# Kernel tuning notes

Measured on AMD Instinct MI355X. Metric: run time of the kernel, lower is better.

The kernel has to match this reference:

```python
import jax, jax.numpy as jnp
import numpy as np

N_NODES = 50000
N_EDGES = 800000
IN_DIM = 256
OUT_DIM = 256


def setup_inputs() -> dict:
    key = jax.random.key(0)
    k_feat, k_src, k_dst, k_w0, k_w1, k_b = jax.random.split(key, 6)
    feat = jax.random.normal(k_feat, (N_NODES, IN_DIM), dtype=jnp.float32)
    src = jax.random.randint(k_src, (N_EDGES,), 0, N_NODES, dtype=jnp.int64)
    dst = jax.random.randint(k_dst, (N_EDGES,), 0, N_NODES, dtype=jnp.int64)
    # GraphConv weights (Glorot-ish scale) and biases
    W0 = jax.random.normal(k_w0, (IN_DIM, OUT_DIM), dtype=jnp.float32) / np.sqrt(IN_DIM)
    W1 = jax.random.normal(k_w1, (OUT_DIM, OUT_DIM), dtype=jnp.float32) / np.sqrt(OUT_DIM)
    b0 = jnp.zeros((OUT_DIM,), dtype=jnp.float32)
    b1 = jnp.zeros((OUT_DIM,), dtype=jnp.float32)
    # single shared nn.PReLU parameter (torch default init 0.25)
    prelu_a = jnp.asarray(0.25, dtype=jnp.float32)
    return {"feat": feat, "src": src, "dst": dst,
            "W0": W0, "b0": b0, "W1": W1, "b1": b1, "prelu_a": prelu_a}


def _prelu(x, a):
    return jnp.where(x >= 0, x, a * x)


def reference(feat, src, dst, W0, b0, W1, b1, prelu_a):
    N = feat.shape[0]
    ones = jnp.ones((src.shape[0],), dtype=feat.dtype)
    out_deg = jnp.zeros((N,), dtype=feat.dtype).at[src].add(ones)
    in_deg = jnp.zeros((N,), dtype=feat.dtype).at[dst].add(ones)
    # DGL norm='both': clamp degrees to >=1 before rsqrt
    norm_s = jax.lax.rsqrt(jnp.maximum(out_deg, 1.0))[:, None]  # [N,1]
    norm_d = jax.lax.rsqrt(jnp.maximum(in_deg, 1.0))[:, None]   # [N,1]

    def graph_conv(h, W, b):
        # h' = D_in^{-1/2} A (D_out^{-1/2} h) W + b
        msg = (h * norm_s)[src]                                   # [E, d]
        agg = jax.ops.segment_sum(msg, dst, num_segments=N)       # [N, d]
        return (agg * norm_d) @ W + b

    h = _prelu(graph_conv(feat, W0, b0), prelu_a)
    hg = jnp.sum(h, axis=0, keepdims=True)                        # SumPooling [1, d]
    h = _prelu(graph_conv(h, W1, b1), prelu_a)
    hg = jnp.concatenate([hg, jnp.sum(h, axis=0, keepdims=True)], axis=-1)
    return (h, hg)
```

## Files before the change

kernel.cpp:

```cpp
#include <hip/hip_runtime.h>
#include <stdint.h>

#define NN 50000
#define NE 800000
#define DIM 256

#define HB 128
#define HT 512
#define HALF 25000
#define HWORDS 12500

#define NSLICE 8
#define SCH 32
#define NPB 64
#define ECH 2048

#define GB ((NN + 31) / 32)

typedef __bf16 bf16x8 __attribute__((ext_vector_type(8)));
typedef float f32x4 __attribute__((ext_vector_type(4)));
typedef unsigned u32x4 __attribute__((ext_vector_type(4)));
typedef int i32x4 __attribute__((ext_vector_type(4)));

__device__ __forceinline__ unsigned short f2bf(float f) {
  union { float f; unsigned u; } v; v.f = f;
  unsigned r = v.u + 0x7fffu + ((v.u >> 16) & 1u);
  return (unsigned short)(r >> 16);
}

__global__ __launch_bounds__(HT) void hist_kernel(const int* __restrict__ src,
                                                  const int* __restrict__ dst,
                                                  unsigned* __restrict__ Hs,
                                                  unsigned* __restrict__ Hd) {
  __shared__ unsigned lds[HWORDS];
  const int tid = threadIdx.x;
  const int b = blockIdx.x;
#pragma unroll
  for (int phase = 0; phase < 4; ++phase) {
    const int* arr = (phase < 2) ? src : dst;
    unsigned* H = (phase < 2) ? Hs : Hd;
    const int r = phase & 1;
    const int lo = r * HALF;
    for (int w = tid; w < HWORDS; w += HT) lds[w] = 0u;
    __syncthreads();
    for (int e = b * HT + tid; e < NE; e += HB * HT) {
      unsigned local = (unsigned)(arr[e] - lo);
      if (local < (unsigned)HALF)
        atomicAdd(&lds[local >> 1], 1u << ((local & 1) * 16));
    }
    __syncthreads();
    for (int w = tid; w < HWORDS; w += HT)
      H[(size_t)b * HALF + r * HWORDS + w] = lds[w];
    __syncthreads();
  }
}

__global__ void reduce_norm_kernel(const unsigned* __restrict__ Hs,
                                   const unsigned* __restrict__ Hd,
                                   unsigned* __restrict__ Pd,
                                   int* __restrict__ in_cnt,
                                   float* __restrict__ norm_s,
                                   float* __restrict__ norm_d,
                                   float* __restrict__ hg) {
  int w = blockIdx.x * blockDim.x + threadIdx.x;
  if (blockIdx.x == 0) {
    hg[threadIdx.x] = 0.f;
    hg[256 + threadIdx.x] = 0.f;
  }
  if (w >= 2 * HWORDS) return;
  unsigned ss = 0, dd = 0;
  for (int b = 0; b < HB; ++b) {
    Pd[(size_t)b * HALF + w] = dd;
    ss += Hs[(size_t)b * HALF + w];
    dd += Hd[(size_t)b * HALF + w];
  }
  int r = (w >= HWORDS) ? 1 : 0;
  int lw = w - r * HWORDS;
  int n0 = r * HALF + lw * 2;
  unsigned s0 = ss & 0xffffu, s1 = ss >> 16;
  unsigned d0 = dd & 0xffffu, d1 = dd >> 16;
  in_cnt[n0] = (int)d0;
  in_cnt[n0 + 1] = (int)d1;
  norm_s[n0] = rsqrtf(fmaxf((float)s0, 1.0f));
  norm_s[n0 + 1] = rsqrtf(fmaxf((float)s1, 1.0f));
  norm_d[n0] = rsqrtf(fmaxf((float)d0, 1.0f));
  norm_d[n0 + 1] = rsqrtf(fmaxf((float)d1, 1.0f));
}

__global__ __launch_bounds__(1024) void scan_kernel(const int* __restrict__ in_cnt,
                                                    int* __restrict__ row_ptr) {
  __shared__ int wsum[16];
  int tid = threadIdx.x;
  int lane = tid & 63, wave = tid >> 6;
  int carry = 0;
  for (int base = 0; base < NN; base += 4096) {
    int i0 = base + tid * 4;
    int v[4];
#pragma unroll
    for (int j = 0; j < 4; ++j) {
      int i = i0 + j;
      v[j] = (i < NN) ? in_cnt[i] : 0;
    }
    int tsum = v[0] + v[1] + v[2] + v[3];
    int incl = tsum;
#pragma unroll
    for (int off = 1; off < 64; off <<= 1) {
      int t = __shfl_up(incl, off, 64);
      if (lane >= off) incl += t;
    }
    if (lane == 63) wsum[wave] = incl;
    __syncthreads();
    int waveoff = 0;
    for (int w = 0; w < wave; ++w) waveoff += wsum[w];
    int chunk_total = 0;
    for (int w = 0; w < 16; ++w) chunk_total += wsum[w];
    int run = carry + waveoff + (incl - tsum);
#pragma unroll
    for (int j = 0; j < 4; ++j) {
      int i = i0 + j;
      if (i < NN) row_ptr[i] = run;
      run += v[j];
    }
    carry += chunk_total;
    __syncthreads();
  }
  if (tid == 0) row_ptr[NN] = carry;
}

__global__ __launch_bounds__(HT) void fill_kernel(const int* __restrict__ src,
                                                  const int* __restrict__ dst,
                                                  const int* __restrict__ row_ptr,
                                                  const unsigned* __restrict__ Pd,
                                                  int* __restrict__ colx) {
  __shared__ unsigned lds[HWORDS];
  const int tid = threadIdx.x;
  const int b = blockIdx.x;
#pragma unroll
  for (int r = 0; r < 2; ++r) {
    const int lo = r * HALF;
    for (int w = tid; w < HWORDS; w += HT) lds[w] = 0u;
    __syncthreads();
    for (int e = b * HT + tid; e < NE; e += HB * HT) {
      int n = dst[e];
      unsigned local = (unsigned)(n - lo);
      if (local < (unsigned)HALF) {
        int sh = (local & 1) * 16;
        unsigned old = atomicAdd(&lds[local >> 1], 1u << sh);
        unsigned rank = (old >> sh) & 0xffffu;
        unsigned pref = (Pd[(size_t)b * HALF + r * HWORDS + (local >> 1)] >> sh) & 0xffffu;
        colx[row_ptr[n] + (int)pref + (int)rank] = src[e];
      }
    }
    __syncthreads();
  }
}

__device__ __forceinline__ void swizzleW_body(const float* __restrict__ W,
                                              unsigned short* __restrict__ Wb, int idx) {
  int lane = idx & 63;
  int blk = idx >> 6;
  int kc = blk & 7, nt = blk >> 3;
  int kbase = kc * 32 + (lane >> 4) * 8;
  int col = nt * 16 + (lane & 15);
  ushort4 o0, o1;
  o0.x = f2bf(W[(size_t)(kbase + 0) * DIM + col]);
  o0.y = f2bf(W[(size_t)(kbase + 1) * DIM + col]);
  o0.z = f2bf(W[(size_t)(kbase + 2) * DIM + col]);
  o0.w = f2bf(W[(size_t)(kbase + 3) * DIM + col]);
  o1.x = f2bf(W[(size_t)(kbase + 4) * DIM + col]);
  o1.y = f2bf(W[(size_t)(kbase + 5) * DIM + col]);
  o1.z = f2bf(W[(size_t)(kbase + 6) * DIM + col]);
  o1.w = f2bf(W[(size_t)(kbase + 7) * DIM + col]);
  ((ushort4*)Wb)[idx * 2 + 0] = o0;
  ((ushort4*)Wb)[idx * 2 + 1] = o1;
}

__global__ void prep_kernel(const float* __restrict__ feat, const float* __restrict__ norm_s,
                            unsigned short* __restrict__ featb,
                            const float* __restrict__ W0, unsigned short* __restrict__ Wb0,
                            const float* __restrict__ W1, unsigned short* __restrict__ Wb1) {
  int blk = blockIdx.x;
  if (blk < 12500) {
    int i = blk * 256 + threadIdx.x;
    int node = i >> 6;
    int ch4 = i & 63;
    float s = norm_s[node];
    float4 v = ((const float4*)feat)[i];
    ushort4 o;
    o.x = f2bf(v.x * s); o.y = f2bf(v.y * s); o.z = f2bf(v.z * s); o.w = f2bf(v.w * s);
    int sl = ch4 >> 3;
    int w4 = ch4 & 7;
    ((ushort4*)featb)[(size_t)sl * (NN * 8) + (size_t)node * 8 + w4] = o;
  } else if (blk < 12532) {
    swizzleW_body(W0, Wb0, (blk - 12500) * 256 + threadIdx.x);
  } else {
    swizzleW_body(W1, Wb1, (blk - 12532) * 256 + threadIdx.x);
  }
}

__device__ __forceinline__ void acc_row(float* a, u32x4 p) {
  a[0] += __uint_as_float(p.x << 16);
  a[1] += __uint_as_float(p.x & 0xffff0000u);
  a[2] += __uint_as_float(p.y << 16);
  a[3] += __uint_as_float(p.y & 0xffff0000u);
  a[4] += __uint_as_float(p.z << 16);
  a[5] += __uint_as_float(p.z & 0xffff0000u);
  a[6] += __uint_as_float(p.w << 16);
  a[7] += __uint_as_float(p.w & 0xffff0000u);
}

__global__ __launch_bounds__(256) void agg_kernel(const unsigned short* __restrict__ X,
                                                  unsigned short* __restrict__ agg,
                                                  const int* __restrict__ row_ptr,
                                                  const int* __restrict__ colx,
                                                  const float* __restrict__ norm_d) {
  __shared__ int ecol[ECH];
  const int s = blockIdx.x & (NSLICE - 1);
  const int nb = blockIdx.x >> 3;
  const int tid = threadIdx.x;
  const int grp = tid >> 2;
  const int cl = tid & 3;
  const int node = nb * NPB + grp;

  const int nfirst = nb * NPB;
  const int nlast = (nfirst + NPB < NN) ? (nfirst + NPB) : NN;
  const int estart = row_ptr[nfirst];
  const int eend = row_ptr[nlast];

  int e = 0, end = 0;
  if (node < NN) { e = row_ptr[node]; end = row_ptr[node + 1]; }

  const unsigned short* Xs = X + (size_t)s * (NN * SCH);
  const size_t loff = (size_t)cl * 8;

  float a[8];
#pragma unroll
  for (int j = 0; j < 8; ++j) a[j] = 0.f;

  const int base0 = estart & ~3;
  for (int base = base0; base < eend; base += ECH) {
    const int lim = (base + ECH < eend) ? (base + ECH) : eend;
    __syncthreads();
    for (int k = base + tid * 4; k < lim; k += 1024) {
      i32x4 v = __builtin_nontemporal_load((const i32x4*)(colx + k));
      *(i32x4*)&ecol[k - base] = v;
    }
    __syncthreads();
    const int hi = (end < lim) ? end : lim;
    for (; e + 4 <= hi; e += 4) {
      int c0 = ecol[e - base + 0];
      int c1 = ecol[e - base + 1];
      int c2 = ecol[e - base + 2];
      int c3 = ecol[e - base + 3];
      u32x4 r0 = *(const u32x4*)(Xs + (size_t)c0 * SCH + loff);
      u32x4 r1 = *(const u32x4*)(Xs + (size_t)c1 * SCH + loff);
      u32x4 r2 = *(const u32x4*)(Xs + (size_t)c2 * SCH + loff);
      u32x4 r3 = *(const u32x4*)(Xs + (size_t)c3 * SCH + loff);
      acc_row(a, r0);
      acc_row(a, r1);
      acc_row(a, r2);
      acc_row(a, r3);
    }
    for (; e < hi; ++e) {
      int c = ecol[e - base];
      u32x4 r = *(const u32x4*)(Xs + (size_t)c * SCH + loff);
      acc_row(a, r);
    }
  }

  if (node < NN) {
    float nd = norm_d[node];
    u32x4 o;
    o.x = (unsigned)f2bf(a[0] * nd) | ((unsigned)f2bf(a[1] * nd) << 16);
    o.y = (unsigned)f2bf(a[2] * nd) | ((unsigned)f2bf(a[3] * nd) << 16);
    o.z = (unsigned)f2bf(a[4] * nd) | ((unsigned)f2bf(a[5] * nd) << 16);
    o.w = (unsigned)f2bf(a[6] * nd) | ((unsigned)f2bf(a[7] * nd) << 16);
    __builtin_nontemporal_store(o, (u32x4*)(agg + (size_t)node * DIM + (size_t)s * SCH + loff));
  }
}

#define LDSROW 264
#define FROW 260
__global__ __launch_bounds__(256) void gemm_mfma_kernel(const unsigned short* __restrict__ A,
                                                        const unsigned short* __restrict__ Wb,
                                                        const float* __restrict__ bias,
                                                        const float* __restrict__ prelu_a_ptr,
                                                        const float* __restrict__ norm_s,
                                                        float* __restrict__ C,
                                                        unsigned short* __restrict__ Cb,
                                                        float* __restrict__ hg_part) {
  __shared__ unsigned short As[32 * LDSROW];
  int tid = threadIdx.x;
  int r0 = blockIdx.x * 32;
#pragma unroll
  for (int p = 0; p < 4; ++p) {
    int idx = p * 256 + tid;
    int row = idx >> 5;
    int seg = idx & 31;
    int grow = r0 + row;
    ushort4 v0 = {0, 0, 0, 0}, v1 = {0, 0, 0, 0};
    if (grow < NN) {
      const ushort4* g = (const ushort4*)(A + (size_t)grow * DIM + seg * 8);
      v0 = g[0]; v1 = g[1];
    }
    *(ushort4*)(&As[row * LDSROW + seg * 8 + 0]) = v0;
    *(ushort4*)(&As[row * LDSROW + seg * 8 + 4]) = v1;
  }
  __syncthreads();

  int wave = tid >> 6, lane = tid & 63;
  int quad = lane >> 4, l16 = lane & 15;

  f32x4 acc[2][4];
#pragma unroll
  for (int mt = 0; mt < 2; ++mt)
#pragma unroll
    for (int nti = 0; nti < 4; ++nti)
      acc[mt][nti] = (f32x4){0.f, 0.f, 0.f, 0.f};

#pragma unroll
  for (int kc = 0; kc < 8; ++kc) {
    bf16x8 a[2], b[4];
#pragma unroll
    for (int mt = 0; mt < 2; ++mt)
      a[mt] = *(const bf16x8*)(&As[(mt * 16 + l16) * LDSROW + kc * 32 + quad * 8]);
#pragma unroll
    for (int nti = 0; nti < 4; ++nti) {
      int nt = wave * 4 + nti;
      b[nti] = *(const bf16x8*)(Wb + ((size_t)(nt * 8 + kc) * 64 + lane) * 8);
    }
#pragma unroll
    for (int mt = 0; mt < 2; ++mt)
#pragma unroll
      for (int nti = 0; nti < 4; ++nti)
        acc[mt][nti] = __builtin_amdgcn_mfma_f32_16x16x32_bf16(a[mt], b[nti], acc[mt][nti], 0, 0, 0);
  }

  float pa = *prelu_a_ptr;
  float bv[4], cs[4];
#pragma unroll
  for (int nti = 0; nti < 4; ++nti) {
    bv[nti] = bias[wave * 64 + nti * 16 + l16];
    cs[nti] = 0.f;
  }
#pragma unroll
  for (int mt = 0; mt < 2; ++mt) {
#pragma unroll
    for (int nti = 0; nti < 4; ++nti) {
#pragma unroll
      for (int r = 0; r < 4; ++r) {
        int rowg = r0 + mt * 16 + quad * 4 + r;
        float x = acc[mt][nti][r] + bv[nti];
        x = (x >= 0.f) ? x : pa * x;
        acc[mt][nti][r] = x;
        if (rowg < NN) cs[nti] += x;
      }
    }
  }
#pragma unroll
  for (int nti = 0; nti < 4; ++nti) {
    cs[nti] += __shfl_xor(cs[nti], 16, 64);
    cs[nti] += __shfl_xor(cs[nti], 32, 64);
  }
  if (quad == 0) {
#pragma unroll
    for (int nti = 0; nti < 4; ++nti)
      hg_part[(size_t)blockIdx.x * 256 + wave * 64 + nti * 16 + l16] = cs[nti];
  }

  float* LF = (float*)As;
#pragma unroll
  for (int chunk = 0; chunk < 2; ++chunk) {
    __syncthreads();
#pragma unroll
    for (int nti = 0; nti < 4; ++nti) {
      int colw = wave * 64 + nti * 16 + l16;
#pragma unroll
      for (int r = 0; r < 4; ++r)
        LF[(quad * 4 + r) * FROW + colw] = acc[chunk][nti][r];
    }
    __syncthreads();
    int rowbase = r0 + chunk * 16;
    if (C) {
#pragma unroll
      for (int s = 0; s < 4; ++s) {
        int g = s * 256 + tid;
        int row = g >> 6, cg = g & 63;
        int rowg = rowbase + row;
        if (rowg < NN) {
          float4 v = *(const float4*)&LF[row * FROW + cg * 4];
          *(float4*)(C + (size_t)rowg * DIM + cg * 4) = v;
        }
      }
    }
    if (Cb) {
#pragma unroll
      for (int s = 0; s < 2; ++s) {
        int g = s * 256 + tid;
        int row = g >> 5, cg = g & 31;
        int rowg = rowbase + row;
        if (rowg < NN) {
          float ns = norm_s[rowg];
          float4 v0 = *(const float4*)&LF[row * FROW + cg * 8];
          float4 v1 = *(const float4*)&LF[row * FROW + cg * 8 + 4];
          uint4 o;
          o.x = (unsigned)f2bf(v0.x * ns) | ((unsigned)f2bf(v0.y * ns) << 16);
          o.y = (unsigned)f2bf(v0.z * ns) | ((unsigned)f2bf(v0.w * ns) << 16);
          o.z = (unsigned)f2bf(v1.x * ns) | ((unsigned)f2bf(v1.y * ns) << 16);
          o.w = (unsigned)f2bf(v1.z * ns) | ((unsigned)f2bf(v1.w * ns) << 16);
          unsigned short* outp = Cb + (size_t)(cg >> 2) * (NN * SCH)
                               + (size_t)rowg * SCH + (size_t)(cg & 3) * 8;
          *(uint4*)outp = o;
        }
      }
    }
  }
}

__global__ __launch_bounds__(256) void hg_reduce_kernel(const float* __restrict__ hg_part,
                                                        float* __restrict__ hg) {
  const int layer = blockIdx.x >> 3;
  const int chunk = blockIdx.x & 7;
  const int c = threadIdx.x;
  const float* base = hg_part + (size_t)layer * GB * 256;
  const int per = (GB + 7) / 8;
  int b0 = chunk * per;
  int b1 = (b0 + per < GB) ? (b0 + per) : GB;
  float s0 = 0.f, s1 = 0.f, s2 = 0.f, s3 = 0.f;
  int b = b0;
  for (; b + 4 <= b1; b += 4) {
    s0 += base[(size_t)(b + 0) * 256 + c];
    s1 += base[(size_t)(b + 1) * 256 + c];
    s2 += base[(size_t)(b + 2) * 256 + c];
    s3 += base[(size_t)(b + 3) * 256 + c];
  }
  for (; b < b1; ++b) s0 += base[(size_t)b * 256 + c];
  atomicAdd(&hg[layer * 256 + c], (s0 + s1) + (s2 + s3));
}

extern "C" void kernel_launch(void* const* d_in, const int* in_sizes, int n_in,
                              void* d_out, int out_size, void* d_ws, size_t ws_size,
                              hipStream_t stream) {
  const float* feat = (const float*)d_in[0];
  const int* src    = (const int*)d_in[1];
  const int* dst    = (const int*)d_in[2];
  const float* W0   = (const float*)d_in[3];
  const float* b0   = (const float*)d_in[4];
  const float* W1   = (const float*)d_in[5];
  const float* b1   = (const float*)d_in[6];
  const float* pa   = (const float*)d_in[7];

  float* out_h = (float*)d_out;
  float* hg    = out_h + (size_t)NN * DIM;

  char* w = (char*)d_ws;
  int* in_cnt   = (int*)w;        w += (size_t)NN * 4;
  float* norm_s = (float*)w;      w += (size_t)NN * 4;
  float* norm_d = (float*)w;      w += (size_t)NN * 4;
  int* row_ptr  = (int*)w;        w += (size_t)(NN + 16) * 4;
  int* colx     = (int*)w;        w += (size_t)(NE + 4) * 4;
  unsigned short* Wb0 = (unsigned short*)w;  w += (size_t)DIM * DIM * 2;
  unsigned short* Wb1 = (unsigned short*)w;  w += (size_t)DIM * DIM * 2;
  float* hg_part = (float*)w;     w += (size_t)2 * GB * 256 * 4;
  uintptr_t ap = ((uintptr_t)w + 255) & ~(uintptr_t)255;
  unsigned short* featb = (unsigned short*)ap;
  unsigned short* aggb  = featb + (size_t)NN * DIM;
  unsigned* Hs = (unsigned*)featb;
  unsigned* Hd = Hs + (size_t)HB * HALF;
  unsigned* Pd = (unsigned*)aggb;

  const int agg_blocks = NSLICE * ((NN + NPB - 1) / NPB);

  hist_kernel<<<HB, HT, 0, stream>>>(src, dst, Hs, Hd);
  reduce_norm_kernel<<<(2 * HWORDS + 255) / 256, 256, 0, stream>>>(Hs, Hd, Pd, in_cnt,
                                                                   norm_s, norm_d, hg);
  prep_kernel<<<12564, 256, 0, stream>>>(feat, norm_s, featb, W0, Wb0, W1, Wb1);
  scan_kernel<<<1, 1024, 0, stream>>>(in_cnt, row_ptr);
  fill_kernel<<<HB, HT, 0, stream>>>(src, dst, row_ptr, Pd, colx);

  agg_kernel<<<agg_blocks, 256, 0, stream>>>(featb, aggb, row_ptr, colx, norm_d);
  gemm_mfma_kernel<<<GB, 256, 0, stream>>>(aggb, Wb0, b0, pa, norm_s,
                                           (float*)nullptr, featb, hg_part);

  agg_kernel<<<agg_blocks, 256, 0, stream>>>(featb, aggb, row_ptr, colx, norm_d);
  gemm_mfma_kernel<<<GB, 256, 0, stream>>>(aggb, Wb1, b1, pa, norm_s,
                                           out_h, (unsigned short*)nullptr, hg_part + (size_t)GB * 256);

  hg_reduce_kernel<<<16, 256, 0, stream>>>(hg_part, hg);
}
```

Baseline: 356.9 us.

## Use full-range LDS histograms, pre-shifted column offsets and wider unrolled aggregation

The histogram and fill kernels now keep one 25000-word LDS array that covers all nodes, so the two-range passes and their range checks go away and each edge array is read fewer times. The fill kernel stores src<<6 as a byte offset, which lets the aggregation kernel form gather addresses with a single OR instead of a multiply and add. The aggregation inner loop is unrolled to 8 gathers in flight, and accumulation uses float2 vectors so the compiler can emit packed adds. The cost is 100KB of LDS per block, which lowers occupancy for the histogram and fill kernels.

```diff
diff --git a/kernel.cpp b/kernel.cpp
--- a/kernel.cpp
+++ b/kernel.cpp
@@ -19,6 +19,7 @@
 
 typedef __bf16 bf16x8 __attribute__((ext_vector_type(8)));
 typedef float f32x4 __attribute__((ext_vector_type(4)));
+typedef float f32x2 __attribute__((ext_vector_type(2)));
 typedef unsigned u32x4 __attribute__((ext_vector_type(4)));
 typedef int i32x4 __attribute__((ext_vector_type(4)));
 
@@ -32,25 +33,22 @@
                                                   const int* __restrict__ dst,
                                                   unsigned* __restrict__ Hs,
                                                   unsigned* __restrict__ Hd) {
-  __shared__ unsigned lds[HWORDS];
+  __shared__ unsigned lds[HALF];
   const int tid = threadIdx.x;
   const int b = blockIdx.x;
 #pragma unroll
-  for (int phase = 0; phase < 4; ++phase) {
-    const int* arr = (phase < 2) ? src : dst;
-    unsigned* H = (phase < 2) ? Hs : Hd;
-    const int r = phase & 1;
-    const int lo = r * HALF;
-    for (int w = tid; w < HWORDS; w += HT) lds[w] = 0u;
+  for (int phase = 0; phase < 2; ++phase) {
+    const int* arr = phase ? dst : src;
+    unsigned* H = phase ? Hd : Hs;
+    for (int w = tid; w < HALF; w += HT) lds[w] = 0u;
     __syncthreads();
     for (int e = b * HT + tid; e < NE; e += HB * HT) {
-      unsigned local = (unsigned)(arr[e] - lo);
-      if (local < (unsigned)HALF)
-        atomicAdd(&lds[local >> 1], 1u << ((local & 1) * 16));
-    }
-    __syncthreads();
-    for (int w = tid; w < HWORDS; w += HT)
-      H[(size_t)b * HALF + r * HWORDS + w] = lds[w];
+      unsigned n = (unsigned)arr[e];
+      atomicAdd(&lds[n >> 1], 1u << ((n & 1) * 16));
+    }
+    __syncthreads();
+    for (int w = tid; w < HALF; w += HT)
+      H[(size_t)b * HALF + w] = lds[w];
     __syncthreads();
   }
 }
@@ -74,9 +72,7 @@
     ss += Hs[(size_t)b * HALF + w];
     dd += Hd[(size_t)b * HALF + w];
   }
-  int r = (w >= HWORDS) ? 1 : 0;
-  int lw = w - r * HWORDS;
-  int n0 = r * HALF + lw * 2;
+  int n0 = w * 2;
   unsigned s0 = ss & 0xffffu, s1 = ss >> 16;
   unsigned d0 = dd & 0xffffu, d1 = dd >> 16;
   in_cnt[n0] = (int)d0;
@@ -132,26 +128,18 @@
                                                   const int* __restrict__ row_ptr,
                                                   const unsigned* __restrict__ Pd,
                                                   int* __restrict__ colx) {
-  __shared__ unsigned lds[HWORDS];
+  __shared__ unsigned lds[HALF];
   const int tid = threadIdx.x;
   const int b = blockIdx.x;
-#pragma unroll
-  for (int r = 0; r < 2; ++r) {
-    const int lo = r * HALF;
-    for (int w = tid; w < HWORDS; w += HT) lds[w] = 0u;
-    __syncthreads();
-    for (int e = b * HT + tid; e < NE; e += HB * HT) {
-      int n = dst[e];
-      unsigned local = (unsigned)(n - lo);
-      if (local < (unsigned)HALF) {
-        int sh = (local & 1) * 16;
-        unsigned old = atomicAdd(&lds[local >> 1], 1u << sh);
-        unsigned rank = (old >> sh) & 0xffffu;
-        unsigned pref = (Pd[(size_t)b * HALF + r * HWORDS + (local >> 1)] >> sh) & 0xffffu;
-        colx[row_ptr[n] + (int)pref + (int)rank] = src[e];
-      }
-    }
-    __syncthreads();
+  for (int w = tid; w < HALF; w += HT) lds[w] = 0u;
+  __syncthreads();
+  for (int e = b * HT + tid; e < NE; e += HB * HT) {
+    int n = dst[e];
+    int sh = (n & 1) * 16;
+    unsigned old = atomicAdd(&lds[n >> 1], 1u << sh);
+    unsigned rank = (old >> sh) & 0xffffu;
+    unsigned pref = (Pd[(size_t)b * HALF + (n >> 1)] >> sh) & 0xffffu;
+    colx[row_ptr[n] + (int)pref + (int)rank] = src[e] << 6;
   }
 }
 
@@ -198,15 +186,15 @@
   }
 }
 
-__device__ __forceinline__ void acc_row(float* a, u32x4 p) {
-  a[0] += __uint_as_float(p.x << 16);
-  a[1] += __uint_as_float(p.x & 0xffff0000u);
-  a[2] += __uint_as_float(p.y << 16);
-  a[3] += __uint_as_float(p.y & 0xffff0000u);
-  a[4] += __uint_as_float(p.z << 16);
-  a[5] += __uint_as_float(p.z & 0xffff0000u);
-  a[6] += __uint_as_float(p.w << 16);
-  a[7] += __uint_as_float(p.w & 0xffff0000u);
+__device__ __forceinline__ void acc_row(f32x2* a, u32x4 p) {
+  f32x2 v0 = { __uint_as_float(p.x << 16), __uint_as_float(p.x & 0xffff0000u) };
+  a[0] += v0;
+  f32x2 v1 = { __uint_as_float(p.y << 16), __uint_as_float(p.y & 0xffff0000u) };
+  a[1] += v1;
+  f32x2 v2 = { __uint_as_float(p.z << 16), __uint_as_float(p.z & 0xffff0000u) };
+  a[2] += v2;
+  f32x2 v3 = { __uint_as_float(p.w << 16), __uint_as_float(p.w & 0xffff0000u) };
+  a[3] += v3;
 }
 
 __global__ __launch_bounds__(256) void agg_kernel(const unsigned short* __restrict__ X,
@@ -230,12 +218,12 @@
   int e = 0, end = 0;
   if (node < NN) { e = row_ptr[node]; end = row_ptr[node + 1]; }
 
-  const unsigned short* Xs = X + (size_t)s * (NN * SCH);
-  const size_t loff = (size_t)cl * 8;
-
-  float a[8];
-#pragma unroll
-  for (int j = 0; j < 8; ++j) a[j] = 0.f;
+  const char* Xp = (const char*)(X + (size_t)s * (NN * SCH));
+  const int lsub = cl * 16;
+
+  f32x2 a[4];
+#pragma unroll
+  for (int j = 0; j < 4; ++j) a[j] = (f32x2){0.f, 0.f};
 
   const int base0 = estart & ~3;
   for (int base = base0; base < eend; base += ECH) {
@@ -247,23 +235,32 @@
     }
     __syncthreads();
     const int hi = (end < lim) ? end : lim;
-    for (; e + 4 <= hi; e += 4) {
-      int c0 = ecol[e - base + 0];
-      int c1 = ecol[e - base + 1];
-      int c2 = ecol[e - base + 2];
-      int c3 = ecol[e - base + 3];
-      u32x4 r0 = *(const u32x4*)(Xs + (size_t)c0 * SCH + loff);
-      u32x4 r1 = *(const u32x4*)(Xs + (size_t)c1 * SCH + loff);
-      u32x4 r2 = *(const u32x4*)(Xs + (size_t)c2 * SCH + loff);
-      u32x4 r3 = *(const u32x4*)(Xs + (size_t)c3 * SCH + loff);
-      acc_row(a, r0);
-      acc_row(a, r1);
-      acc_row(a, r2);
-      acc_row(a, r3);
+    for (; e + 8 <= hi; e += 8) {
+      int o_[8];
+#pragma unroll
+      for (int j = 0; j < 8; ++j) o_[j] = ecol[e - base + j];
+      u32x4 r_[8];
+#pragma unroll
+      for (int j = 0; j < 8; ++j)
+        r_[j] = *(const u32x4*)(Xp + (size_t)(unsigned)(o_[j] | lsub));
+#pragma unroll
+      for (int j = 0; j < 8; ++j) acc_row(a, r_[j]);
+    }
+    if (e + 4 <= hi) {
+      int o_[4];
+#pragma unroll
+      for (int j = 0; j < 4; ++j) o_[j] = ecol[e - base + j];
+      u32x4 r_[4];
+#pragma unroll
+      for (int j = 0; j < 4; ++j)
+        r_[j] = *(const u32x4*)(Xp + (size_t)(unsigned)(o_[j] | lsub));
+#pragma unroll
+      for (int j = 0; j < 4; ++j) acc_row(a, r_[j]);
+      e += 4;
     }
     for (; e < hi; ++e) {
-      int c = ecol[e - base];
-      u32x4 r = *(const u32x4*)(Xs + (size_t)c * SCH + loff);
+      int o0 = ecol[e - base];
+      u32x4 r = *(const u32x4*)(Xp + (size_t)(unsigned)(o0 | lsub));
       acc_row(a, r);
     }
   }
@@ -271,11 +268,11 @@
   if (node < NN) {
     float nd = norm_d[node];
     u32x4 o;
-    o.x = (unsigned)f2bf(a[0] * nd) | ((unsigned)f2bf(a[1] * nd) << 16);
-    o.y = (unsigned)f2bf(a[2] * nd) | ((unsigned)f2bf(a[3] * nd) << 16);
-    o.z = (unsigned)f2bf(a[4] * nd) | ((unsigned)f2bf(a[5] * nd) << 16);
-    o.w = (unsigned)f2bf(a[6] * nd) | ((unsigned)f2bf(a[7] * nd) << 16);
-    __builtin_nontemporal_store(o, (u32x4*)(agg + (size_t)node * DIM + (size_t)s * SCH + loff));
+    o.x = (unsigned)f2bf(a[0].x * nd) | ((unsigned)f2bf(a[0].y * nd) << 16);
+    o.y = (unsigned)f2bf(a[1].x * nd) | ((unsigned)f2bf(a[1].y * nd) << 16);
+    o.z = (unsigned)f2bf(a[2].x * nd) | ((unsigned)f2bf(a[2].y * nd) << 16);
+    o.w = (unsigned)f2bf(a[3].x * nd) | ((unsigned)f2bf(a[3].y * nd) << 16);
+    __builtin_nontemporal_store(o, (u32x4*)(agg + (size_t)node * DIM + (size_t)s * SCH + (size_t)cl * 8));
   }
 }
 
```

New measurement: 353.9 us. About the same (-0.8%).
